# Kernel tuning notes

Measured on AMD Instinct MI355X. Metric: run time of the kernel, lower is better.

The kernel has to match this reference:

```python
import jax, jax.numpy as jnp
import numpy as np

N = 8192      # num nodes
E = 262144    # num edges (avg degree 32)
IN = 512
HID = 512
LAT = 128


def setup_inputs() -> dict:
    key = jax.random.key(0)
    ks = jax.random.split(key, 8)
    edge_index = jax.random.randint(ks[0], (2, E), 0, N, dtype=jnp.int64 if jax.config.read('jax_enable_x64') else jnp.int32)
    x = jax.random.normal(ks[1], (N, IN), jnp.float32)
    def w(k, i, o):
        return jax.random.normal(k, (i, o), jnp.float32) * (1.0 / np.sqrt(i))
    return {
        'edge_index': edge_index,
        'x': x,
        'W1': w(ks[2], IN, HID), 'b1': jnp.zeros((HID,), jnp.float32),
        'Wmu': w(ks[3], HID, LAT), 'bmu': jnp.zeros((LAT,), jnp.float32),
        'Wlv': w(ks[4], HID, LAT), 'blv': jnp.zeros((LAT,), jnp.float32),
    }


def gcn_conv(x, row, col, W, b):
    # PyG GCNConv: h = x W; symmetric norm with self-loops (added by caller);
    # out[i] = sum_{(j->i)} d_j^{-1/2} d_i^{-1/2} h[j] + b
    h = x @ W
    ones = jnp.ones((row.shape[0],), h.dtype)
    deg = jax.ops.segment_sum(ones, col, num_segments=N)  # in-degree incl. self-loop
    dinv_sqrt = jnp.where(deg > 0, jax.lax.rsqrt(jnp.maximum(deg, 1e-12)), 0.0)
    norm = dinv_sqrt[row] * dinv_sqrt[col]                # [E+N]
    out = jax.ops.segment_sum(norm[:, None] * h[row], col, num_segments=N)
    return out + b


def reference(edge_index, x, W1, b1, Wmu, bmu, Wlv, blv):
    # add self-loops once, reuse for all layers
    loops = jnp.arange(N, dtype=edge_index.dtype)
    row = jnp.concatenate([edge_index[0], loops])
    col = jnp.concatenate([edge_index[1], loops])

    h = jax.nn.relu(gcn_conv(x, row, col, W1, b1))
    mu = gcn_conv(h, row, col, Wmu, bmu)
    logvar = gcn_conv(h, row, col, Wlv, blv)
    z = mu  # eval-mode reparameterize (deterministic)
    A_pred = jax.nn.sigmoid(z @ z.T)  # [N, N] dot-product decode
    return (A_pred, mu, logvar, z)
```

## Files before the change

kernel.cpp:

```cpp
#include <hip/hip_runtime.h>

#define NNODES 8192
#define NEDGES 262144
#define FIN 512
#define FHID 512
#define FLAT 128

typedef unsigned short bfu;
typedef __attribute__((ext_vector_type(8))) short short8;
typedef __attribute__((ext_vector_type(4))) float f32x4;

__device__ __forceinline__ float bf2f(unsigned short u) {
    union { unsigned int i; float f; } c; c.i = ((unsigned int)u) << 16; return c.f;
}
__device__ __forceinline__ unsigned short f2bf(float f) {
    union { float f; unsigned int i; } c; c.f = f;
    unsigned int i = c.i;
    unsigned int r = (i + 0x7FFFu + ((i >> 16) & 1u)) >> 16;
    return (unsigned short)r;
}

__global__ void k_zero(int* p, int n) {
    int i = blockIdx.x * blockDim.x + threadIdx.x;
    if (i < n) p[i] = 0;
}

__global__ void k_count(const int* __restrict__ ei, int* __restrict__ deg) {
    int e = blockIdx.x * blockDim.x + threadIdx.x;
    if (e < NEDGES) atomicAdd(&deg[ei[NEDGES + e]], 1);
}

__global__ void k_scan(const int* __restrict__ deg, int* __restrict__ row_start,
                       float* __restrict__ dinv) {
    __shared__ int part[256];
    int t = threadIdx.x, base = t * 32;
    int s = 0;
    for (int i = 0; i < 32; i++) s += deg[base + i];
    part[t] = s;
    __syncthreads();
    for (int off = 1; off < 256; off <<= 1) {
        int v = (t >= off) ? part[t - off] : 0;
        __syncthreads();
        part[t] += v;
        __syncthreads();
    }
    int run = (t == 0) ? 0 : part[t - 1];
    for (int i = 0; i < 32; i++) {
        int d = deg[base + i];
        row_start[base + i] = run;
        run += d;
        dinv[base + i] = rsqrtf((float)(d + 1));
    }
    if (t == 255) row_start[NNODES] = run;
}

__global__ void k_scatter(const int* __restrict__ ei, const int* __restrict__ row_start,
                          int* __restrict__ cursor, int* __restrict__ csr) {
    int e = blockIdx.x * blockDim.x + threadIdx.x;
    if (e < NEDGES) {
        int dst = ei[NEDGES + e];
        int p = atomicAdd(&cursor[dst], 1);
        csr[row_start[dst] + p] = ei[e];
    }
}

__global__ void k_cvt_x(const float* __restrict__ x, bfu* __restrict__ xb) {
    int i = blockIdx.x * blockDim.x + threadIdx.x;
    const float4 v = ((const float4*)x)[i];
    ushort2 lo = {f2bf(v.x), f2bf(v.y)};
    ushort2 hi = {f2bf(v.z), f2bf(v.w)};
    ((ushort2*)xb)[2 * i] = lo;
    ((ushort2*)xb)[2 * i + 1] = hi;
}

__global__ void k_bt(const float* __restrict__ W1, const float* __restrict__ Wmu,
                     const float* __restrict__ Wlv, bfu* __restrict__ Bt1, bfu* __restrict__ Bt2) {
    int idx = blockIdx.x * blockDim.x + threadIdx.x;
    if (idx < 512 * 512) {
        int n = idx >> 9, k = idx & 511;
        Bt1[idx] = f2bf(W1[k * 512 + n]);
    } else if (idx < 512 * 512 + 256 * 512) {
        int j = idx - 512 * 512;
        int n = j >> 9, k = j & 511;
        Bt2[j] = f2bf((n < 128) ? Wmu[k * 128 + n] : Wlv[k * 128 + (n - 128)]);
    }
}

template <int ACT, typename CT>
__global__ void k_gemm_nt(const bfu* __restrict__ A, const bfu* __restrict__ Bt,
                          CT* __restrict__ C, int M, int N, int K) {
    int wid  = (blockIdx.x * blockDim.x + threadIdx.x) >> 6;
    int lane = threadIdx.x & 63;
    int l = lane & 15, q = lane >> 4;
    int tn = N >> 6;
    int m0 = (wid / tn) << 6, n0 = (wid % tn) << 6;

    f32x4 acc[4][4];
#pragma unroll
    for (int a = 0; a < 4; a++)
#pragma unroll
        for (int b = 0; b < 4; b++) acc[a][b] = (f32x4){0.f, 0.f, 0.f, 0.f};

    const bfu* Ap = A + (size_t)(m0 + l) * K + q * 8;
    const bfu* Bp = Bt + (size_t)(n0 + l) * K + q * 8;

    for (int k0 = 0; k0 < K; k0 += 32) {
        short8 av[4], bv[4];
#pragma unroll
        for (int mi = 0; mi < 4; mi++)
            av[mi] = *(const short8*)(Ap + (size_t)mi * 16 * K + k0);
#pragma unroll
        for (int ni = 0; ni < 4; ni++)
            bv[ni] = *(const short8*)(Bp + (size_t)ni * 16 * K + k0);
#pragma unroll
        for (int mi = 0; mi < 4; mi++)
#pragma unroll
            for (int ni = 0; ni < 4; ni++)
                acc[mi][ni] = __builtin_amdgcn_mfma_f32_16x16x32_bf16(av[mi], bv[ni],
                                                                     acc[mi][ni], 0, 0, 0);
    }

#pragma unroll
    for (int mi = 0; mi < 4; mi++)
#pragma unroll
        for (int ni = 0; ni < 4; ni++) {
            int col = n0 + ni * 16 + l;
#pragma unroll
            for (int r = 0; r < 4; r++) {
                int row = m0 + mi * 16 + q * 4 + r;
                float v = acc[mi][ni][r];
                if (ACT == 2) v = 1.0f / (1.0f + __expf(-v));
                if constexpr (sizeof(CT) == 2)
                    C[(size_t)row * N + col] = (CT)f2bf(v);
                else
                    C[(size_t)row * N + col] = (CT)v;
            }
        }
}

__global__ void k_agg1(const bfu* __restrict__ hin, const int* __restrict__ csr,
                       const int* __restrict__ rs, const float* __restrict__ dinv,
                       const float* __restrict__ bias, bfu* __restrict__ hout) {
    int i = blockIdx.x;
    int f = threadIdx.x * 2;
    float a0 = 0.f, a1 = 0.f;
    int s = rs[i], e = rs[i + 1];
    for (int ed = s; ed < e; ed++) {
        int src = csr[ed];
        float w = dinv[src];
        unsigned int pk = *(const unsigned int*)(hin + (size_t)src * FHID + f);
        a0 += w * bf2f((unsigned short)(pk & 0xFFFF));
        a1 += w * bf2f((unsigned short)(pk >> 16));
    }
    float di = dinv[i];
    unsigned int pk = *(const unsigned int*)(hin + (size_t)i * FHID + f);
    a0 += di * bf2f((unsigned short)(pk & 0xFFFF));
    a1 += di * bf2f((unsigned short)(pk >> 16));
    float o0 = fmaxf(di * a0 + bias[f], 0.f);
    float o1 = fmaxf(di * a1 + bias[f + 1], 0.f);
    unsigned int outw = (unsigned int)f2bf(o0) | ((unsigned int)f2bf(o1) << 16);
    *(unsigned int*)(hout + (size_t)i * FHID + f) = outw;
}

__global__ void k_agg2(const bfu* __restrict__ hin, const int* __restrict__ csr,
                       const int* __restrict__ rs, const float* __restrict__ dinv,
                       const float* __restrict__ bmu, const float* __restrict__ blv,
                       float* __restrict__ out_mu, float* __restrict__ out_lv,
                       float* __restrict__ out_z, bfu* __restrict__ ws_z) {
    int i = blockIdx.x;
    int f = threadIdx.x * 2;
    float a0 = 0.f, a1 = 0.f;
    int s = rs[i], e = rs[i + 1];
    for (int ed = s; ed < e; ed++) {
        int src = csr[ed];
        float w = dinv[src];
        unsigned int pk = *(const unsigned int*)(hin + (size_t)src * 256 + f);
        a0 += w * bf2f((unsigned short)(pk & 0xFFFF));
        a1 += w * bf2f((unsigned short)(pk >> 16));
    }
    float di = dinv[i];
    unsigned int pk = *(const unsigned int*)(hin + (size_t)i * 256 + f);
    a0 += di * bf2f((unsigned short)(pk & 0xFFFF));
    a1 += di * bf2f((unsigned short)(pk >> 16));
    float v0 = di * a0, v1 = di * a1;
    if (f < 128) {
        v0 += bmu[f]; v1 += bmu[f + 1];
        float2 fv = {v0, v1};
        *(float2*)(out_mu + (size_t)i * FLAT + f) = fv;
        *(float2*)(out_z + (size_t)i * FLAT + f) = fv;
        unsigned int bw = (unsigned int)f2bf(v0) | ((unsigned int)f2bf(v1) << 16);
        *(unsigned int*)(ws_z + (size_t)i * FLAT + f) = bw;
    } else {
        int fl = f - 128;
        v0 += blv[fl]; v1 += blv[fl + 1];
        float2 fv = {v0, v1};
        *(float2*)(out_lv + (size_t)i * FLAT + fl) = fv;
    }
}

extern "C" void kernel_launch(void* const* d_in, const int* in_sizes, int n_in,
                              void* d_out, int out_size, void* d_ws, size_t ws_size,
                              hipStream_t stream) {
    const int*   ei  = (const int*)d_in[0];
    const float* x   = (const float*)d_in[1];
    const float* W1  = (const float*)d_in[2];
    const float* b1  = (const float*)d_in[3];
    const float* Wmu = (const float*)d_in[4];
    const float* bmu = (const float*)d_in[5];
    const float* Wlv = (const float*)d_in[6];
    const float* blv = (const float*)d_in[7];
    float* out = (float*)d_out;

    char* wsb = (char*)d_ws;
    size_t off = 0;
    auto alloc = [&](size_t bytes) -> char* {
        char* p = wsb + off;
        off += (bytes + 255) & ~(size_t)255;
        return p;
    };
    int*   deg       = (int*)alloc(NNODES * 4);
    int*   cursor    = (int*)alloc(NNODES * 4);
    int*   row_start = (int*)alloc((NNODES + 1) * 4);
    float* dinv      = (float*)alloc(NNODES * 4);
    int*   csr       = (int*)alloc(NEDGES * 4);
    bfu*   Bt1       = (bfu*)alloc(512 * 512 * 2);
    bfu*   Bt2       = (bfu*)alloc(256 * 512 * 2);
    bfu*   xb        = (bfu*)alloc((size_t)NNODES * FIN * 2);
    bfu*   h0        = (bfu*)alloc((size_t)NNODES * FHID * 2);
    bfu*   h         = (bfu*)alloc((size_t)NNODES * FHID * 2);
    bfu*   hml       = (bfu*)alloc((size_t)NNODES * 256 * 2);
    bfu*   zb        = (bfu*)alloc((size_t)NNODES * FLAT * 2);

    float* out_mu = out + (size_t)NNODES * NNODES;
    float* out_lv = out_mu + (size_t)NNODES * FLAT;
    float* out_z  = out_lv + (size_t)NNODES * FLAT;

    k_zero<<<(2 * NNODES + 255) / 256, 256, 0, stream>>>(deg, 2 * NNODES);
    k_count<<<NEDGES / 256, 256, 0, stream>>>(ei, deg);
    k_scan<<<1, 256, 0, stream>>>(deg, row_start, dinv);
    k_scatter<<<NEDGES / 256, 256, 0, stream>>>(ei, row_start, cursor, csr);
    k_bt<<<(512 * 512 + 256 * 512) / 256, 256, 0, stream>>>(W1, Wmu, Wlv, Bt1, Bt2);
    k_cvt_x<<<(NNODES * FIN / 4) / 256, 256, 0, stream>>>(x, xb);

    k_gemm_nt<0, bfu><<<(8192 / 64) * (512 / 64) / 4, 256, 0, stream>>>(xb, Bt1, h0, 8192, 512, 512);
    k_agg1<<<NNODES, 256, 0, stream>>>(h0, csr, row_start, dinv, b1, h);

    k_gemm_nt<0, bfu><<<(8192 / 64) * (256 / 64) / 4, 256, 0, stream>>>(h, Bt2, hml, 8192, 256, 512);
    k_agg2<<<NNODES, 128, 0, stream>>>(hml, csr, row_start, dinv, bmu, blv,
                                       out_mu, out_lv, out_z, zb);

    k_gemm_nt<2, float><<<(8192 / 64) * (8192 / 64) / 4, 256, 0, stream>>>(zb, zb, out, 8192, 8192, 128);
}
```

Measured before the change: 517.2 us.

## Vectorize GEMM epilogue stores, precompute edge weights, unroll aggregation, retile small GEMMs

Measured after the change: 478.5 us. 1.08x faster.

```diff
diff --git a/kernel.cpp b/kernel.cpp
--- a/kernel.cpp
+++ b/kernel.cpp
@@ -9,6 +9,7 @@
 typedef unsigned short bfu;
 typedef __attribute__((ext_vector_type(8))) short short8;
 typedef __attribute__((ext_vector_type(4))) float f32x4;
+typedef __attribute__((ext_vector_type(4))) unsigned short us4;
 
 __device__ __forceinline__ float bf2f(unsigned short u) {
     union { unsigned int i; float f; } c; c.i = ((unsigned int)u) << 16; return c.f;
@@ -64,6 +65,12 @@
     }
 }
 
+__global__ void k_wcsr(const int* __restrict__ csr, const float* __restrict__ dinv,
+                       float* __restrict__ wcsr) {
+    int p = blockIdx.x * blockDim.x + threadIdx.x;
+    if (p < NEDGES) wcsr[p] = dinv[csr[p]];
+}
+
 __global__ void k_cvt_x(const float* __restrict__ x, bfu* __restrict__ xb) {
     int i = blockIdx.x * blockDim.x + threadIdx.x;
     const float4 v = ((const float4*)x)[i];
@@ -86,76 +93,107 @@
     }
 }
 
-template <int ACT, typename CT>
+template <int ACT, int TM, int TN, typename CT>
 __global__ void k_gemm_nt(const bfu* __restrict__ A, const bfu* __restrict__ Bt,
                           CT* __restrict__ C, int M, int N, int K) {
     int wid  = (blockIdx.x * blockDim.x + threadIdx.x) >> 6;
     int lane = threadIdx.x & 63;
     int l = lane & 15, q = lane >> 4;
-    int tn = N >> 6;
-    int m0 = (wid / tn) << 6, n0 = (wid % tn) << 6;
-
-    f32x4 acc[4][4];
-#pragma unroll
-    for (int a = 0; a < 4; a++)
-#pragma unroll
-        for (int b = 0; b < 4; b++) acc[a][b] = (f32x4){0.f, 0.f, 0.f, 0.f};
+    int tn = N / (16 * TN);
+    int m0 = (wid / tn) * (16 * TM), n0 = (wid % tn) * (16 * TN);
+
+    f32x4 acc[TM][TN];
+#pragma unroll
+    for (int a = 0; a < TM; a++)
+#pragma unroll
+        for (int b = 0; b < TN; b++) acc[a][b] = (f32x4){0.f, 0.f, 0.f, 0.f};
 
     const bfu* Ap = A + (size_t)(m0 + l) * K + q * 8;
     const bfu* Bp = Bt + (size_t)(n0 + l) * K + q * 8;
 
     for (int k0 = 0; k0 < K; k0 += 32) {
-        short8 av[4], bv[4];
-#pragma unroll
-        for (int mi = 0; mi < 4; mi++)
+        short8 av[TM], bv[TN];
+#pragma unroll
+        for (int mi = 0; mi < TM; mi++)
             av[mi] = *(const short8*)(Ap + (size_t)mi * 16 * K + k0);
 #pragma unroll
-        for (int ni = 0; ni < 4; ni++)
+        for (int ni = 0; ni < TN; ni++)
             bv[ni] = *(const short8*)(Bp + (size_t)ni * 16 * K + k0);
 #pragma unroll
-        for (int mi = 0; mi < 4; mi++)
-#pragma unroll
-            for (int ni = 0; ni < 4; ni++)
-                acc[mi][ni] = __builtin_amdgcn_mfma_f32_16x16x32_bf16(av[mi], bv[ni],
+        for (int mi = 0; mi < TM; mi++)
+#pragma unroll
+            for (int ni = 0; ni < TN; ni++)
+                acc[mi][ni] = __builtin_amdgcn_mfma_f32_16x16x32_bf16(bv[ni], av[mi],
                                                                      acc[mi][ni], 0, 0, 0);
     }
 
 #pragma unroll
-    for (int mi = 0; mi < 4; mi++)
-#pragma unroll
-        for (int ni = 0; ni < 4; ni++) {
-            int col = n0 + ni * 16 + l;
-#pragma unroll
-            for (int r = 0; r < 4; r++) {
-                int row = m0 + mi * 16 + q * 4 + r;
-                float v = acc[mi][ni][r];
-                if (ACT == 2) v = 1.0f / (1.0f + __expf(-v));
-                if constexpr (sizeof(CT) == 2)
-                    C[(size_t)row * N + col] = (CT)f2bf(v);
-                else
-                    C[(size_t)row * N + col] = (CT)v;
+    for (int mi = 0; mi < TM; mi++) {
+        int row = m0 + mi * 16 + l;
+#pragma unroll
+        for (int ni = 0; ni < TN; ni++) {
+            int col = n0 + ni * 16 + q * 4;
+            f32x4 v = acc[mi][ni];
+            if (ACT == 2) {
+#pragma unroll
+                for (int r = 0; r < 4; r++)
+                    v[r] = __builtin_amdgcn_rcpf(1.0f + __expf(-v[r]));
+            }
+            if constexpr (sizeof(CT) == 2) {
+                us4 o = {f2bf(v[0]), f2bf(v[1]), f2bf(v[2]), f2bf(v[3])};
+                *(us4*)(C + (size_t)row * N + col) = o;
+            } else {
+                *(f32x4*)(C + (size_t)row * N + col) = v;
             }
         }
+    }
+}
+
+template <int F>
+__device__ __forceinline__ void agg_core(const bfu* __restrict__ hin,
+                                         const int* __restrict__ csr,
+                                         const float* __restrict__ wcsr,
+                                         int s, int e, int i, int f, float di,
+                                         float& a0, float& a1) {
+    a0 = 0.f; a1 = 0.f;
+    int ed = s;
+    for (; ed + 4 <= e; ed += 4) {
+        int s0 = csr[ed], s1 = csr[ed + 1], s2 = csr[ed + 2], s3 = csr[ed + 3];
+        float w0 = wcsr[ed], w1 = wcsr[ed + 1], w2 = wcsr[ed + 2], w3 = wcsr[ed + 3];
+        unsigned int p0 = *(const unsigned int*)(hin + (size_t)s0 * F + f);
+        unsigned int p1 = *(const unsigned int*)(hin + (size_t)s1 * F + f);
+        unsigned int p2 = *(const unsigned int*)(hin + (size_t)s2 * F + f);
+        unsigned int p3 = *(const unsigned int*)(hin + (size_t)s3 * F + f);
+        a0 += w0 * bf2f((unsigned short)(p0 & 0xFFFF));
+        a1 += w0 * bf2f((unsigned short)(p0 >> 16));
+        a0 += w1 * bf2f((unsigned short)(p1 & 0xFFFF));
+        a1 += w1 * bf2f((unsigned short)(p1 >> 16));
+        a0 += w2 * bf2f((unsigned short)(p2 & 0xFFFF));
+        a1 += w2 * bf2f((unsigned short)(p2 >> 16));
+        a0 += w3 * bf2f((unsigned short)(p3 & 0xFFFF));
+        a1 += w3 * bf2f((unsigned short)(p3 >> 16));
+    }
+    for (; ed < e; ed++) {
+        int src = csr[ed];
+        float w = wcsr[ed];
+        unsigned int pk = *(const unsigned int*)(hin + (size_t)src * F + f);
+        a0 += w * bf2f((unsigned short)(pk & 0xFFFF));
+        a1 += w * bf2f((unsigned short)(pk >> 16));
+    }
+    unsigned int pk = *(const unsigned int*)(hin + (size_t)i * F + f);
+    a0 += di * bf2f((unsigned short)(pk & 0xFFFF));
+    a1 += di * bf2f((unsigned short)(pk >> 16));
 }
 
 __global__ void k_agg1(const bfu* __restrict__ hin, const int* __restrict__ csr,
-                       const int* __restrict__ rs, const float* __restrict__ dinv,
-                       const float* __restrict__ bias, bfu* __restrict__ hout) {
+                       const float* __restrict__ wcsr, const int* __restrict__ rs,
+                       const float* __restrict__ dinv, const float* __restrict__ bias,
+                       bfu* __restrict__ hout) {
     int i = blockIdx.x;
     int f = threadIdx.x * 2;
-    float a0 = 0.f, a1 = 0.f;
-    int s = rs[i], e = rs[i + 1];
-    for (int ed = s; ed < e; ed++) {
-        int src = csr[ed];
-        float w = dinv[src];
-        unsigned int pk = *(const unsigned int*)(hin + (size_t)src * FHID + f);
-        a0 += w * bf2f((unsigned short)(pk & 0xFFFF));
-        a1 += w * bf2f((unsigned short)(pk >> 16));
-    }
     float di = dinv[i];
-    unsigned int pk = *(const unsigned int*)(hin + (size_t)i * FHID + f);
-    a0 += di * bf2f((unsigned short)(pk & 0xFFFF));
-    a1 += di * bf2f((unsigned short)(pk >> 16));
+    float a0, a1;
+    agg_core<FHID>(hin, csr, wcsr, rs[i], rs[i + 1], i, f, di, a0, a1);
     float o0 = fmaxf(di * a0 + bias[f], 0.f);
     float o1 = fmaxf(di * a1 + bias[f + 1], 0.f);
     unsigned int outw = (unsigned int)f2bf(o0) | ((unsigned int)f2bf(o1) << 16);
@@ -163,25 +201,16 @@
 }
 
 __global__ void k_agg2(const bfu* __restrict__ hin, const int* __restrict__ csr,
-                       const int* __restrict__ rs, const float* __restrict__ dinv,
-                       const float* __restrict__ bmu, const float* __restrict__ blv,
-                       float* __restrict__ out_mu, float* __restrict__ out_lv,
-                       float* __restrict__ out_z, bfu* __restrict__ ws_z) {
+                       const float* __restrict__ wcsr, const int* __restrict__ rs,
+                       const float* __restrict__ dinv, const float* __restrict__ bmu,
+                       const float* __restrict__ blv, float* __restrict__ out_mu,
+                       float* __restrict__ out_lv, float* __restrict__ out_z,
+                       bfu* __restrict__ ws_z) {
     int i = blockIdx.x;
     int f = threadIdx.x * 2;
-    float a0 = 0.f, a1 = 0.f;
-    int s = rs[i], e = rs[i + 1];
-    for (int ed = s; ed < e; ed++) {
-        int src = csr[ed];
-        float w = dinv[src];
-        unsigned int pk = *(const unsigned int*)(hin + (size_t)src * 256 + f);
-        a0 += w * bf2f((unsigned short)(pk & 0xFFFF));
-        a1 += w * bf2f((unsigned short)(pk >> 16));
-    }
     float di = dinv[i];
-    unsigned int pk = *(const unsigned int*)(hin + (size_t)i * 256 + f);
-    a0 += di * bf2f((unsigned short)(pk & 0xFFFF));
-    a1 += di * bf2f((unsigned short)(pk >> 16));
+    float a0, a1;
+    agg_core<256>(hin, csr, wcsr, rs[i], rs[i + 1], i, f, di, a0, a1);
     float v0 = di * a0, v1 = di * a1;
     if (f < 128) {
         v0 += bmu[f]; v1 += bmu[f + 1];
@@ -223,6 +252,7 @@
     int*   row_start = (int*)alloc((NNODES + 1) * 4);
     float* dinv      = (float*)alloc(NNODES * 4);
     int*   csr       = (int*)alloc(NEDGES * 4);
+    float* wcsr      = (float*)alloc(NEDGES * 4);
     bfu*   Bt1       = (bfu*)alloc(512 * 512 * 2);
     bfu*   Bt2       = (bfu*)alloc(256 * 512 * 2);
     bfu*   xb        = (bfu*)alloc((size_t)NNODES * FIN * 2);
@@ -239,15 +269,19 @@
     k_count<<<NEDGES / 256, 256, 0, stream>>>(ei, deg);
     k_scan<<<1, 256, 0, stream>>>(deg, row_start, dinv);
     k_scatter<<<NEDGES / 256, 256, 0, stream>>>(ei, row_start, cursor, csr);
+    k_wcsr<<<NEDGES / 256, 256, 0, stream>>>(csr, dinv, wcsr);
     k_bt<<<(512 * 512 + 256 * 512) / 256, 256, 0, stream>>>(W1, Wmu, Wlv, Bt1, Bt2);
     k_cvt_x<<<(NNODES * FIN / 4) / 256, 256, 0, stream>>>(x, xb);
 
-    k_gemm_nt<0, bfu><<<(8192 / 64) * (512 / 64) / 4, 256, 0, stream>>>(xb, Bt1, h0, 8192, 512, 512);
-    k_agg1<<<NNODES, 256, 0, stream>>>(h0, csr, row_start, dinv, b1, h);
-
-    k_gemm_nt<0, bfu><<<(8192 / 64) * (256 / 64) / 4, 256, 0, stream>>>(h, Bt2, hml, 8192, 256, 512);
-    k_agg2<<<NNODES, 128, 0, stream>>>(hml, csr, row_start, dinv, bmu, blv,
+    k_gemm_nt<0, 4, 2, bfu><<<(8192 / 64) * (512 / 32) / 4, 256, 0, stream>>>(
+        xb, Bt1, h0, 8192, 512, 512);
+    k_agg1<<<NNODES, 256, 0, stream>>>(h0, csr, wcsr, row_start, dinv, b1, h);
+
+    k_gemm_nt<0, 2, 2, bfu><<<(8192 / 32) * (256 / 32) / 4, 256, 0, stream>>>(
+        h, Bt2, hml, 8192, 256, 512);
+    k_agg2<<<NNODES, 128, 0, stream>>>(hml, csr, wcsr, row_start, dinv, bmu, blv,
                                        out_mu, out_lv, out_z, zb);
 
-    k_gemm_nt<2, float><<<(8192 / 64) * (8192 / 64) / 4, 256, 0, stream>>>(zb, zb, out, 8192, 8192, 128);
-}
+    k_gemm_nt<2, 4, 4, float><<<(8192 / 64) * (8192 / 64) / 4, 256, 0, stream>>>(
+        zb, zb, out, 8192, 8192, 128);
+}
```
